# Optimization experiments

Measured on AMD Instinct MI355X. Metric: run time of the kernel, lower is better.

## Reference

```python
import jax, jax.numpy as jnp
import numpy as np

S, H, NH, DS = 4096, 1024, 2, 64   # seq_len, hidden, num_heads, static_in_size
HD = H // NH                        # head_dim = 512
EPS = 1e-5                          # eqx.nn.LayerNorm default eps


def setup_inputs() -> dict:
    key = jax.random.key(0)
    ks = jax.random.split(key, 11)
    sc = lambda n: 1.0 / np.sqrt(n)
    return {
        "inputs": jax.random.normal(ks[0], (S, H), jnp.float32),
        "static_data": jax.random.normal(ks[1], (DS,), jnp.float32),
        "base_mask": jax.random.randint(ks[2], (S,), 0, 2).astype(bool),
        "Wq": jax.random.normal(ks[3], (H, H), jnp.float32) * sc(H),
        "Wk": jax.random.normal(ks[4], (H, H), jnp.float32) * sc(H),
        "Wv": jax.random.normal(ks[5], (H, H), jnp.float32) * sc(H),
        "Wo": jax.random.normal(ks[6], (H, H), jnp.float32) * sc(H),
        "Ws": jax.random.normal(ks[7], (H, DS), jnp.float32) * sc(DS),
        "bs": jax.random.normal(ks[8], (H,), jnp.float32) * 0.01,
        "ln_w": jnp.ones((H,), jnp.float32),
        "ln_b": jnp.zeros((H,), jnp.float32),
    }


def reference(inputs, static_data, base_mask, Wq, Wk, Wv, Wo, Ws, bs, ln_w, ln_b):
    # static embedding injected into keys/values
    semb = Ws @ static_data + bs                      # [H]
    kv_in = inputs + semb[None, :]                    # [S, H]

    # per-head projections (eqx Linear: y = W @ x, no bias in MHA projections)
    q = (inputs @ Wq.T).reshape(S, NH, HD)
    k = (kv_in @ Wk.T).reshape(S, NH, HD)
    v = (kv_in @ Wv.T).reshape(S, NH, HD)

    logits = jnp.einsum('qhd,khd->hqk', q, k) / np.sqrt(HD)  # [NH, S, S]

    # head 0: irregular mask (base_mask broadcast over queries); head 1: all-ones
    irregular = jnp.broadcast_to(base_mask[None, :], (S, S))
    mask = jnp.stack([irregular, jnp.ones((S, S), bool)], axis=0)  # [2, S, S]
    logits = jnp.where(mask, logits, jnp.finfo(logits.dtype).min)

    attn = jax.nn.softmax(logits, axis=-1)
    ctx = jnp.einsum('hqk,khd->qhd', attn, v).reshape(S, H)
    out = ctx @ Wo.T                                  # output projection

    # dropout_rate = 0 -> identity; residual + per-token LayerNorm
    res = out + inputs
    mu = res.mean(-1, keepdims=True)
    var = res.var(-1, keepdims=True)
    return (res - mu) / jnp.sqrt(var + EPS) * ln_w + ln_b
```

## Files before the change

kernel.cpp:

```cpp
#include <hip/hip_runtime.h>
#include <stdint.h>

#define S_LEN  4096
#define HID    1024
#define NHEAD  2
#define HDIM   512
#define NSPLIT 4
#define KS_STRIDE 520
#define LN_EPS 1e-5f

typedef __bf16 bf16x8 __attribute__((ext_vector_type(8)));
typedef float  f32x4  __attribute__((ext_vector_type(4)));

__device__ __forceinline__ float b2f(unsigned short u) {
    return __uint_as_float(((unsigned int)u) << 16);
}
__device__ __forceinline__ unsigned short f2b(float f) {
    unsigned int u = __float_as_uint(f);
    u += 0x7FFFu + ((u >> 16) & 1u);
    return (unsigned short)(u >> 16);
}

__device__ __forceinline__ void async_cp16(const void* g, void* l) {
    __builtin_amdgcn_global_load_lds(
        (const __attribute__((address_space(1))) unsigned int*)g,
        (__attribute__((address_space(3))) unsigned int*)l, 16, 0, 0);
}

__global__ void k_cvt4s(const float* __restrict__ i0, const float* __restrict__ i1,
                        const float* __restrict__ i2, const float* __restrict__ i3,
                        unsigned short* __restrict__ o0, unsigned short* __restrict__ o1,
                        unsigned short* __restrict__ o2, unsigned short* __restrict__ o3,
                        const float* __restrict__ Ws, const float* __restrict__ sd,
                        const float* __restrict__ bs, float* __restrict__ semb) {
    int z = blockIdx.y;
    if (z == 4) {
        int j = blockIdx.x * blockDim.x + threadIdx.x;
        if (j >= HID) return;
        float acc = bs[j];
        const float* row = Ws + j * 64;
        #pragma unroll
        for (int d = 0; d < 64; ++d) acc += row[d] * sd[d];
        semb[j] = acc;
        return;
    }
    const float* in = z == 0 ? i0 : z == 1 ? i1 : z == 2 ? i2 : i3;
    unsigned short* o = z == 0 ? o0 : z == 1 ? o1 : z == 2 ? o2 : o3;
    int i = (blockIdx.x * blockDim.x + threadIdx.x) * 8;
    float4 a = *(const float4*)(in + i);
    float4 b = *(const float4*)(in + i + 4);
    unsigned short r[8] = {f2b(a.x), f2b(a.y), f2b(a.z), f2b(a.w),
                           f2b(b.x), f2b(b.y), f2b(b.z), f2b(b.w)};
    *(uint4*)(o + i) = *(const uint4*)r;
}

__global__ void k_kvin(const float* __restrict__ X,
                       const float* __restrict__ semb,
                       unsigned short* __restrict__ Xb,
                       unsigned short* __restrict__ kv) {
    int idx = (blockIdx.x * blockDim.x + threadIdx.x) * 8;
    if (idx >= S_LEN * HID) return;
    int col = idx & (HID - 1);
    float4 a = *(const float4*)(X + idx);
    float4 b = *(const float4*)(X + idx + 4);
    unsigned short xo[8] = {f2b(a.x), f2b(a.y), f2b(a.z), f2b(a.w),
                            f2b(b.x), f2b(b.y), f2b(b.z), f2b(b.w)};
    *(uint4*)(Xb + idx) = *(const uint4*)xo;
    unsigned short o[8];
    o[0] = f2b(a.x + semb[col + 0]);
    o[1] = f2b(a.y + semb[col + 1]);
    o[2] = f2b(a.z + semb[col + 2]);
    o[3] = f2b(a.w + semb[col + 3]);
    o[4] = f2b(b.x + semb[col + 4]);
    o[5] = f2b(b.y + semb[col + 5]);
    o[6] = f2b(b.z + semb[col + 6]);
    o[7] = f2b(b.w + semb[col + 7]);
    *(uint4*)(kv + idx) = *(const uint4*)o;
}

__device__ __forceinline__
void gemm128(const unsigned short* __restrict__ A,
             const unsigned short* __restrict__ B,
             unsigned short* __restrict__ Cb,
             int nx, int ldc) {
    __shared__ unsigned short As[128 * 32];
    __shared__ unsigned short Bs[128 * 32];
    int tid  = threadIdx.x;
    int wave = tid >> 6, lane = tid & 63;
    int quad = lane >> 4, l16 = lane & 15;
    int wm = wave >> 1, wn = wave & 1;
    int m0 = (blockIdx.x / nx) * 128, n0 = (blockIdx.x % nx) * 128;

    f32x4 zero = {0.f, 0.f, 0.f, 0.f};
    f32x4 acc[4][4];
    #pragma unroll
    for (int i = 0; i < 4; ++i)
        #pragma unroll
        for (int j = 0; j < 4; ++j) acc[i][j] = zero;

    for (int k0 = 0; k0 < HID; k0 += 32) {
        #pragma unroll
        for (int i = 0; i < 2; ++i) {
            int c = tid + i * 256;
            async_cp16(A + (m0 + (c >> 2)) * HID + k0 + (c & 3) * 8, As + c * 8);
            async_cp16(B + (n0 + (c >> 2)) * HID + k0 + (c & 3) * 8, Bs + c * 8);
        }
        __syncthreads();
        bf16x8 af[4], bfr[4];
        #pragma unroll
        for (int i = 0; i < 4; ++i)
            af[i] = *(const bf16x8*)(As + (wm * 64 + i * 16 + l16) * 32 + quad * 8);
        #pragma unroll
        for (int j = 0; j < 4; ++j)
            bfr[j] = *(const bf16x8*)(Bs + (wn * 64 + j * 16 + l16) * 32 + quad * 8);
        #pragma unroll
        for (int i = 0; i < 4; ++i)
            #pragma unroll
            for (int j = 0; j < 4; ++j)
                acc[i][j] = __builtin_amdgcn_mfma_f32_16x16x32_bf16(af[i], bfr[j], acc[i][j], 0, 0, 0);
        __syncthreads();
    }

    #pragma unroll
    for (int i = 0; i < 4; ++i) {
        int rbase = m0 + wm * 64 + i * 16 + quad * 4;
        #pragma unroll
        for (int j = 0; j < 4; ++j) {
            int col = n0 + wn * 64 + j * 16 + l16;
            #pragma unroll
            for (int r = 0; r < 4; ++r)
                Cb[(size_t)(rbase + r) * ldc + col] = f2b(acc[i][j][r]);
        }
    }
}

__global__ __launch_bounds__(256)
void k_gemm_qkv(const unsigned short* __restrict__ Xb,
                const unsigned short* __restrict__ kvin,
                const unsigned short* __restrict__ Wqb,
                const unsigned short* __restrict__ Wkb,
                const unsigned short* __restrict__ Wvb,
                unsigned short* __restrict__ Qb,
                unsigned short* __restrict__ Kb,
                unsigned short* __restrict__ Vt) {
    int z = blockIdx.z;
    if (z == 0)      gemm128(Xb,   Wqb,  Qb,  8, HID);
    else if (z == 1) gemm128(kvin, Wkb,  Kb,  8, HID);
    else             gemm128(Wvb,  kvin, Vt, 32, S_LEN);
}

__global__ __launch_bounds__(256)
void k_gemm_o(const unsigned short* __restrict__ A,
              const unsigned short* __restrict__ B,
              float* __restrict__ Cf,
              const float* __restrict__ Xres) {
    __shared__ unsigned short As[64 * 32];
    __shared__ unsigned short Bs[128 * 32];
    int tid  = threadIdx.x;
    int wave = tid >> 6, lane = tid & 63;
    int quad = lane >> 4, l16 = lane & 15;
    int m0 = (blockIdx.x >> 3) * 64, n0 = (blockIdx.x & 7) * 128;

    f32x4 zero = {0.f, 0.f, 0.f, 0.f};
    f32x4 acc[4][2];
    #pragma unroll
    for (int i = 0; i < 4; ++i)
        #pragma unroll
        for (int j = 0; j < 2; ++j) acc[i][j] = zero;

    for (int k0 = 0; k0 < HID; k0 += 32) {
        async_cp16(A + (m0 + (tid >> 2)) * HID + k0 + (tid & 3) * 8, As + tid * 8);
        #pragma unroll
        for (int i = 0; i < 2; ++i) {
            int c = tid + i * 256;
            async_cp16(B + (n0 + (c >> 2)) * HID + k0 + (c & 3) * 8, Bs + c * 8);
        }
        __syncthreads();
        bf16x8 af[4], bfr[2];
        #pragma unroll
        for (int i = 0; i < 4; ++i)
            af[i] = *(const bf16x8*)(As + (i * 16 + l16) * 32 + quad * 8);
        #pragma unroll
        for (int j = 0; j < 2; ++j)
            bfr[j] = *(const bf16x8*)(Bs + (wave * 32 + j * 16 + l16) * 32 + quad * 8);
        #pragma unroll
        for (int i = 0; i < 4; ++i)
            #pragma unroll
            for (int j = 0; j < 2; ++j)
                acc[i][j] = __builtin_amdgcn_mfma_f32_16x16x32_bf16(af[i], bfr[j], acc[i][j], 0, 0, 0);
        __syncthreads();
    }

    #pragma unroll
    for (int i = 0; i < 4; ++i) {
        int rbase = m0 + i * 16 + quad * 4;
        #pragma unroll
        for (int j = 0; j < 2; ++j) {
            int col = n0 + wave * 32 + j * 16 + l16;
            #pragma unroll
            for (int r = 0; r < 4; ++r) {
                size_t o = (size_t)(rbase + r) * HID + col;
                Cf[o] = acc[i][j][r] + Xres[o];
            }
        }
    }
}

__global__ __launch_bounds__(256, 2)
void k_flash(const unsigned short* __restrict__ Q,
             const unsigned short* __restrict__ K,
             const unsigned short* __restrict__ Vt,
             const int* __restrict__ mask,
             unsigned short* __restrict__ Opart,
             float* __restrict__ Lbuf) {
    __shared__ unsigned short Ks[2][32 * KS_STRIDE];
    __shared__ __bf16 Ps[64][40];
    int tid  = threadIdx.x;
    int wave = tid >> 6, lane = tid & 63;
    int quad = lane >> 4, l16 = lane & 15;
    int head = blockIdx.x / NSPLIT, split = blockIdx.x % NSPLIT, qtile = blockIdx.y;

    int qrow = qtile * 64 + wave * 16 + l16;
    const unsigned short* qp = Q + qrow * HID + head * HDIM;
    bf16x8 qf[16];
    #pragma unroll
    for (int t = 0; t < 16; ++t) qf[t] = *(const bf16x8*)(qp + t * 32 + quad * 8);

    float lsum[4];
    #pragma unroll
    for (int r = 0; r < 4; ++r) lsum[r] = 0.f;
    f32x4 zero = {0.f, 0.f, 0.f, 0.f};
    f32x4 oacc[4][8];
    #pragma unroll
    for (int mt = 0; mt < 4; ++mt)
        #pragma unroll
        for (int nt = 0; nt < 8; ++nt) oacc[mt][nt] = zero;

    const float scale = 0.044194173824159216f;
    const unsigned short* Kbase = K + head * HDIM;
    const unsigned short* Vbase = Vt + (size_t)(head * HDIM + wave * 128) * S_LEN;

    {
        int k0 = split * 1024;
        #pragma unroll
        for (int i = 0; i < 8; ++i) {
            int c = tid + i * 256;
            int row = c >> 6, col = (c & 63) * 8;
            async_cp16(Kbase + (k0 + row) * HID + col, Ks[0] + row * KS_STRIDE + col);
        }
    }

    int cur = 0;
    for (int it = 0; it < 32; ++it) {
        int k0 = split * 1024 + it * 32;
        __syncthreads();

        bf16x8 vfe[4];
        #pragma unroll
        for (int nt = 0; nt < 4; ++nt)
            vfe[nt] = *(const bf16x8*)(Vbase + (size_t)(nt * 16 + l16) * S_LEN + k0 + quad * 8);

        f32x4 sacc[2];
        sacc[0] = zero; sacc[1] = zero;
        #pragma unroll
        for (int nt = 0; nt < 2; ++nt)
            #pragma unroll
            for (int t = 0; t < 16; ++t) {
                bf16x8 kf = *(const bf16x8*)(Ks[cur] + (nt * 16 + l16) * KS_STRIDE + t * 32 + quad * 8);
                sacc[nt] = __builtin_amdgcn_mfma_f32_16x16x32_bf16(qf[t], kf, sacc[nt], 0, 0, 0);
            }

        bool keep0 = (head != 0) || (mask[k0 + l16] != 0);
        bool keep1 = (head != 0) || (mask[k0 + 16 + l16] != 0);

        #pragma unroll
        for (int r = 0; r < 4; ++r) {
            float p0 = keep0 ? __expf(fminf(sacc[0][r] * scale, 30.f)) : 0.f;
            float p1 = keep1 ? __expf(fminf(sacc[1][r] * scale, 30.f)) : 0.f;
            lsum[r] += p0 + p1;
            Ps[wave * 16 + quad * 4 + r][l16]      = (__bf16)p0;
            Ps[wave * 16 + quad * 4 + r][16 + l16] = (__bf16)p1;
        }
        __syncthreads();

        if (it < 31) {
            int kn = k0 + 32;
            #pragma unroll
            for (int i = 0; i < 8; ++i) {
                int c = tid + i * 256;
                int row = c >> 6, col = (c & 63) * 8;
                async_cp16(Kbase + (kn + row) * HID + col, Ks[cur ^ 1] + row * KS_STRIDE + col);
            }
        }

        bf16x8 pf[4];
        #pragma unroll
        for (int mt = 0; mt < 4; ++mt)
            pf[mt] = *(const bf16x8*)&Ps[mt * 16 + l16][quad * 8];
        #pragma unroll
        for (int nt = 0; nt < 8; ++nt) {
            bf16x8 vf = (nt < 4) ? vfe[nt]
                : *(const bf16x8*)(Vbase + (size_t)(nt * 16 + l16) * S_LEN + k0 + quad * 8);
            #pragma unroll
            for (int mt = 0; mt < 4; ++mt)
                oacc[mt][nt] = __builtin_amdgcn_mfma_f32_16x16x32_bf16(pf[mt], vf, oacc[mt][nt], 0, 0, 0);
        }
        cur ^= 1;
    }

    #pragma unroll
    for (int r = 0; r < 4; ++r) {
        float s = lsum[r];
        #pragma unroll
        for (int off = 1; off < 16; off <<= 1)
            s += __shfl_xor(s, off, 64);
        lsum[r] = s;
    }
    int lrow = qtile * 64 + wave * 16 + quad * 4;
    if (l16 == 0) {
        #pragma unroll
        for (int r = 0; r < 4; ++r)
            Lbuf[(split * NHEAD + head) * S_LEN + lrow + r] = lsum[r];
    }
    unsigned short* op = Opart + (size_t)split * S_LEN * HID;
    #pragma unroll
    for (int mt = 0; mt < 4; ++mt)
        #pragma unroll
        for (int nt = 0; nt < 8; ++nt)
            #pragma unroll
            for (int r = 0; r < 4; ++r)
                op[(qtile * 64 + mt * 16 + quad * 4 + r) * HID +
                   head * HDIM + wave * 128 + nt * 16 + l16] = f2b(oacc[mt][nt][r]);
}

__global__ void k_combine(const unsigned short* __restrict__ Opart,
                          const float* __restrict__ Lbuf,
                          unsigned short* __restrict__ ctx) {
    const int SH = S_LEN * HID;
    int idx = blockIdx.x * blockDim.x + threadIdx.x;
    if (idx >= SH) return;
    int s = idx >> 10;
    int h = (idx >> 9) & 1;
    float l = 0.f, v = 0.f;
    #pragma unroll
    for (int z = 0; z < NSPLIT; ++z) {
        l += Lbuf[(z * NHEAD + h) * S_LEN + s];
        v += b2f(Opart[(size_t)z * SH + idx]);
    }
    ctx[idx] = f2b(v / l);
}

__global__ __launch_bounds__(256)
void k_ln(const float* __restrict__ res,
          const float* __restrict__ w,
          const float* __restrict__ b,
          float* __restrict__ out) {
    __shared__ float red[8];
    int s = blockIdx.x, tid = threadIdx.x;
    const float* row = res + s * HID;
    float x[4], s1 = 0.f, s2 = 0.f;
    #pragma unroll
    for (int i = 0; i < 4; ++i) {
        x[i] = row[tid + i * 256];
        s1 += x[i]; s2 += x[i] * x[i];
    }
    #pragma unroll
    for (int off = 1; off < 64; off <<= 1) {
        s1 += __shfl_xor(s1, off, 64);
        s2 += __shfl_xor(s2, off, 64);
    }
    int wave = tid >> 6;
    if ((tid & 63) == 0) { red[wave] = s1; red[4 + wave] = s2; }
    __syncthreads();
    s1 = red[0] + red[1] + red[2] + red[3];
    s2 = red[4] + red[5] + red[6] + red[7];
    float mu   = s1 * (1.f / HID);
    float var  = s2 * (1.f / HID) - mu * mu;
    float rstd = rsqrtf(var + LN_EPS);
    #pragma unroll
    for (int i = 0; i < 4; ++i) {
        int col = tid + i * 256;
        out[s * HID + col] = (x[i] - mu) * rstd * w[col] + b[col];
    }
}

extern "C" void kernel_launch(void* const* d_in, const int* in_sizes, int n_in,
                              void* d_out, int out_size, void* d_ws, size_t ws_size,
                              hipStream_t stream) {
    const float* X   = (const float*)d_in[0];
    const float* sd  = (const float*)d_in[1];
    const int*   msk = (const int*)d_in[2];
    const float* Wq  = (const float*)d_in[3];
    const float* Wk  = (const float*)d_in[4];
    const float* Wv  = (const float*)d_in[5];
    const float* Wo  = (const float*)d_in[6];
    const float* Wsp = (const float*)d_in[7];
    const float* bsp = (const float*)d_in[8];
    const float* lw  = (const float*)d_in[9];
    const float* lb  = (const float*)d_in[10];
    float* out = (float*)d_out;

    char* ws = (char*)d_ws;
    const size_t MB = 1ull << 20;
    float*          semb  = (float*)(ws);
    float*          Lbuf  = (float*)(ws + (1ull << 16));
    unsigned short* Xb    = (unsigned short*)(ws + 1 * MB);
    unsigned short* kvin  = (unsigned short*)(ws + 9 * MB);
    unsigned short* Qb    = (unsigned short*)(ws + 17 * MB);
    unsigned short* Kb    = (unsigned short*)(ws + 25 * MB);
    unsigned short* Vt    = (unsigned short*)(ws + 33 * MB);
    unsigned short* ctx   = (unsigned short*)(ws + 41 * MB);
    unsigned short* Wqb   = (unsigned short*)(ws + 49 * MB);
    unsigned short* Wkb   = (unsigned short*)(ws + 51 * MB);
    unsigned short* Wvb   = (unsigned short*)(ws + 53 * MB);
    unsigned short* Wob   = (unsigned short*)(ws + 55 * MB);
    float*          resf  = (float*)(ws + 17 * MB);
    unsigned short* Opart = (unsigned short*)(ws + 57 * MB);

    const int SH = S_LEN * HID;
    const int WW = HID * HID;

    k_cvt4s<<<dim3(WW / 8 / 256, 5), dim3(256), 0, stream>>>(
        Wq, Wk, Wv, Wo, Wqb, Wkb, Wvb, Wob, Wsp, sd, bsp, semb);

    k_kvin<<<dim3(SH / 8 / 256), dim3(256), 0, stream>>>(X, semb, Xb, kvin);

    k_gemm_qkv<<<dim3(256, 1, 3), dim3(256), 0, stream>>>(Xb, kvin, Wqb, Wkb, Wvb, Qb, Kb, Vt);

    k_flash<<<dim3(NHEAD * NSPLIT, S_LEN / 64), dim3(256), 0, stream>>>(
        Qb, Kb, Vt, msk, Opart, Lbuf);

    k_combine<<<dim3(SH / 256), dim3(256), 0, stream>>>(Opart, Lbuf, ctx);
    k_gemm_o<<<dim3(512), dim3(256), 0, stream>>>(ctx, Wob, resf, X);
    k_ln<<<dim3(S_LEN), dim3(256), 0, stream>>>(resf, lw, lb, out);
}
```

Before: 307.4 us.

## Software-pipeline flash attention: defer PV MFMA one iteration, double-buffer P tile

Restructures the flash-attention loop so the P·V MFMAs for the previous key tile run at the top of the next iteration, alongside the QK^T MFMAs, using a double-buffered P shared-memory tile. One barrier per iteration is dropped, the K prefetch is issued right after the barrier, all V fragments are loaded into registers ahead of use, and mask values are prefetched one tile early. MFMA sections get raised wave priority through s_setprio. The aim is to hide V and mask global-load latency and barrier stalls behind matrix work, at the cost of more live registers (eight V fragments plus the 4x8 accumulators), which may spill or lower occupancy under the 256x2 launch bounds.

```diff
diff --git a/kernel.cpp b/kernel.cpp
--- a/kernel.cpp
+++ b/kernel.cpp
@@ -214,7 +214,7 @@
              unsigned short* __restrict__ Opart,
              float* __restrict__ Lbuf) {
     __shared__ unsigned short Ks[2][32 * KS_STRIDE];
-    __shared__ __bf16 Ps[64][40];
+    __shared__ __bf16 Ps[2][64][40];
     int tid  = threadIdx.x;
     int wave = tid >> 6, lane = tid & 63;
     int quad = lane >> 4, l16 = lane & 15;
@@ -238,27 +238,43 @@
 
     const float scale = 0.044194173824159216f;
     const unsigned short* Kbase = K + head * HDIM;
-    const unsigned short* Vbase = Vt + (size_t)(head * HDIM + wave * 128) * S_LEN;
-
-    {
-        int k0 = split * 1024;
+    const unsigned short* vptr = Vt + (size_t)(head * HDIM + wave * 128 + l16) * S_LEN
+                                    + split * 1024 + quad * 8;
+
+    auto stageK = [&](int kt, int buf) {
+        int kb = split * 1024 + kt * 32;
         #pragma unroll
         for (int i = 0; i < 8; ++i) {
             int c = tid + i * 256;
             int row = c >> 6, col = (c & 63) * 8;
-            async_cp16(Kbase + (k0 + row) * HID + col, Ks[0] + row * KS_STRIDE + col);
-        }
-    }
-
-    int cur = 0;
+            async_cp16(Kbase + (kb + row) * HID + col, &Ks[buf][row * KS_STRIDE + col]);
+        }
+    };
+
+    stageK(0, 0);
+    int mk0 = 1, mk1 = 1;
+    if (head == 0) {
+        mk0 = mask[split * 1024 + l16];
+        mk1 = mask[split * 1024 + 16 + l16];
+    }
+
+    bf16x8 vf[8];
     for (int it = 0; it < 32; ++it) {
-        int k0 = split * 1024 + it * 32;
+        int cur = it & 1;
         __syncthreads();
 
-        bf16x8 vfe[4];
-        #pragma unroll
-        for (int nt = 0; nt < 4; ++nt)
-            vfe[nt] = *(const bf16x8*)(Vbase + (size_t)(nt * 16 + l16) * S_LEN + k0 + quad * 8);
+        if (it < 31) stageK(it + 1, cur ^ 1);
+
+        __builtin_amdgcn_s_setprio(1);
+        if (it > 0) {
+            #pragma unroll
+            for (int mt = 0; mt < 4; ++mt) {
+                bf16x8 pf = *(const bf16x8*)&Ps[cur ^ 1][mt * 16 + l16][quad * 8];
+                #pragma unroll
+                for (int nt = 0; nt < 8; ++nt)
+                    oacc[mt][nt] = __builtin_amdgcn_mfma_f32_16x16x32_bf16(pf, vf[nt], oacc[mt][nt], 0, 0, 0);
+            }
+        }
 
         f32x4 sacc[2];
         sacc[0] = zero; sacc[1] = zero;
@@ -266,46 +282,40 @@
         for (int nt = 0; nt < 2; ++nt)
             #pragma unroll
             for (int t = 0; t < 16; ++t) {
-                bf16x8 kf = *(const bf16x8*)(Ks[cur] + (nt * 16 + l16) * KS_STRIDE + t * 32 + quad * 8);
+                bf16x8 kf = *(const bf16x8*)&Ks[cur][(nt * 16 + l16) * KS_STRIDE + t * 32 + quad * 8];
                 sacc[nt] = __builtin_amdgcn_mfma_f32_16x16x32_bf16(qf[t], kf, sacc[nt], 0, 0, 0);
             }
-
-        bool keep0 = (head != 0) || (mask[k0 + l16] != 0);
-        bool keep1 = (head != 0) || (mask[k0 + 16 + l16] != 0);
-
+        __builtin_amdgcn_s_setprio(0);
+
+        #pragma unroll
+        for (int nt = 0; nt < 8; ++nt)
+            vf[nt] = *(const bf16x8*)(vptr + (size_t)nt * 16 * S_LEN + it * 32);
+
+        bool keep0 = mk0 != 0;
+        bool keep1 = mk1 != 0;
         #pragma unroll
         for (int r = 0; r < 4; ++r) {
             float p0 = keep0 ? __expf(fminf(sacc[0][r] * scale, 30.f)) : 0.f;
             float p1 = keep1 ? __expf(fminf(sacc[1][r] * scale, 30.f)) : 0.f;
             lsum[r] += p0 + p1;
-            Ps[wave * 16 + quad * 4 + r][l16]      = (__bf16)p0;
-            Ps[wave * 16 + quad * 4 + r][16 + l16] = (__bf16)p1;
-        }
-        __syncthreads();
-
-        if (it < 31) {
-            int kn = k0 + 32;
-            #pragma unroll
-            for (int i = 0; i < 8; ++i) {
-                int c = tid + i * 256;
-                int row = c >> 6, col = (c & 63) * 8;
-                async_cp16(Kbase + (kn + row) * HID + col, Ks[cur ^ 1] + row * KS_STRIDE + col);
-            }
-        }
-
-        bf16x8 pf[4];
-        #pragma unroll
-        for (int mt = 0; mt < 4; ++mt)
-            pf[mt] = *(const bf16x8*)&Ps[mt * 16 + l16][quad * 8];
-        #pragma unroll
-        for (int nt = 0; nt < 8; ++nt) {
-            bf16x8 vf = (nt < 4) ? vfe[nt]
-                : *(const bf16x8*)(Vbase + (size_t)(nt * 16 + l16) * S_LEN + k0 + quad * 8);
-            #pragma unroll
-            for (int mt = 0; mt < 4; ++mt)
-                oacc[mt][nt] = __builtin_amdgcn_mfma_f32_16x16x32_bf16(pf[mt], vf, oacc[mt][nt], 0, 0, 0);
-        }
-        cur ^= 1;
+            Ps[cur][wave * 16 + quad * 4 + r][l16]      = (__bf16)p0;
+            Ps[cur][wave * 16 + quad * 4 + r][16 + l16] = (__bf16)p1;
+        }
+
+        if (head == 0 && it < 31) {
+            int kn = split * 1024 + (it + 1) * 32;
+            mk0 = mask[kn + l16];
+            mk1 = mask[kn + 16 + l16];
+        }
+    }
+
+    __syncthreads();
+    #pragma unroll
+    for (int mt = 0; mt < 4; ++mt) {
+        bf16x8 pf = *(const bf16x8*)&Ps[1][mt * 16 + l16][quad * 8];
+        #pragma unroll
+        for (int nt = 0; nt < 8; ++nt)
+            oacc[mt][nt] = __builtin_amdgcn_mfma_f32_16x16x32_bf16(pf, vf[nt], oacc[mt][nt], 0, 0, 0);
     }
 
     #pragma unroll
```

Result: slower. 354.2 us (+15.2%).
